# Performance work log

Measured on AMD Instinct MI355X. Metric: run time of the kernel, lower is better.

The kernel has to match this reference:

```python
import jax, jax.numpy as jnp
import numpy as np

B = 1048576  # number of Gaussians
EPS = 1e-8


def setup_inputs() -> dict:
    key = jax.random.key(0)
    ks = jax.random.split(key, 6)
    return {
        "loc1": jax.random.normal(ks[0], (B, 3), dtype=jnp.float32),
        "scale1": jax.random.uniform(ks[1], (B, 3), dtype=jnp.float32),
        "rot_matrix1": jax.random.normal(ks[2], (B, 3, 3), dtype=jnp.float32),
        "loc2": jax.random.normal(ks[3], (B, 3), dtype=jnp.float32),
        "scale2": jax.random.uniform(ks[4], (B, 3), dtype=jnp.float32),
        "rot_matrix2": jax.random.normal(ks[5], (B, 3, 3), dtype=jnp.float32),
    }


def reference(loc1, scale1, rot_matrix1, loc2, scale2, rot_matrix2):
    # Wasserstein-2 distance between batched 3D Gaussians.
    scale1 = jnp.clip(scale1, EPS)
    scale2 = jnp.clip(scale2, EPS)

    loc_diff2 = jnp.sum((loc1 - loc2) ** 2, axis=-1)  # [B]

    # cov2 = R2 diag(scale2) R2^T  -> [B,3,3]
    cov2 = jnp.einsum('bij,bj,bkj->bik', rot_matrix2, scale2, rot_matrix2)

    # cov2 rotated into frame 1: R1^T cov2 R1
    cov2_R1 = jnp.einsum('bji,bjk,bkl->bil', rot_matrix1, cov2, rot_matrix1)

    # E = diag(sqrt(scale1)) cov2_R1 diag(sqrt(scale1)), symmetrized
    s1_sqrt = jnp.sqrt(scale1)  # [B,3]
    E = s1_sqrt[:, :, None] * cov2_R1 * s1_sqrt[:, None, :]
    E = 0.5 * (E + jnp.swapaxes(E, -1, -2)) + EPS * jnp.eye(3, dtype=E.dtype)

    eigs = jnp.clip(jnp.linalg.eigvalsh(E), EPS)  # [B,3]
    E_sqrt_trace = jnp.sqrt(eigs).sum(axis=-1)  # [B]

    cov_w = (scale1.sum(axis=-1)
             + jnp.einsum('bii->b', cov2)
             - 2.0 * E_sqrt_trace)
    cov_w = jnp.clip(cov_w, 0.0)

    return jnp.sqrt(jnp.clip(loc_diff2 + cov_w, EPS))
```

## Files before the change

kernel.cpp:

```cpp
#include <hip/hip_runtime.h>
#include <math.h>

#define EPSF 1e-8f

__device__ __forceinline__ double tr_sqrt_eig(double a00, double a11, double a22,
                                              double a01, double a02, double a12)
{
    double q = (a00 + a11 + a22) * (1.0 / 3.0);
    double b00 = a00 - q, b11 = a11 - q, b22 = a22 - q;
    double p1 = a01 * a01 + a02 * a02 + a12 * a12;
    double p2 = b00 * b00 + b11 * b11 + b22 * b22 + 2.0 * p1;

    double e0, e1, e2;
    if (p2 <= 1e-30) {
        e0 = q; e1 = q; e2 = q;
    } else {
        double p = sqrt(p2 * (1.0 / 6.0));
        double invp = 1.0 / p;
        double c00 = b00 * invp, c11 = b11 * invp, c22 = b22 * invp;
        double c01 = a01 * invp, c02 = a02 * invp, c12 = a12 * invp;
        double detB = c00 * (c11 * c22 - c12 * c12)
                    - c01 * (c01 * c22 - c12 * c02)
                    + c02 * (c01 * c12 - c11 * c02);
        double r = 0.5 * detB;
        r = fmin(1.0, fmax(-1.0, r));
        double phi = acos(r) * (1.0 / 3.0);
        double twop = 2.0 * p;
        e0 = q + twop * cos(phi);
        e2 = q + twop * cos(phi + 2.0943951023931953);
        e1 = 3.0 * q - e0 - e2;
    }
    double eps_d = 1e-8;
    return sqrt(fmax(e0, eps_d)) + sqrt(fmax(e1, eps_d)) + sqrt(fmax(e2, eps_d));
}

__global__ __launch_bounds__(256) void wasserstein_kernel(
    const float* __restrict__ loc1, const float* __restrict__ scale1,
    const float* __restrict__ rot1, const float* __restrict__ loc2,
    const float* __restrict__ scale2, const float* __restrict__ rot2,
    float* __restrict__ out, int B4)
{
    int t = blockIdx.x * blockDim.x + threadIdx.x;
    if (t >= B4) return;

    const float4* l1p = (const float4*)loc1   + 3 * t;
    const float4* l2p = (const float4*)loc2   + 3 * t;
    const float4* s1p = (const float4*)scale1 + 3 * t;
    const float4* s2p = (const float4*)scale2 + 3 * t;
    const float4* r1p = (const float4*)rot1   + 9 * t;
    const float4* r2p = (const float4*)rot2   + 9 * t;

    float loc_diff2[4];
    {
        float L1[12], L2[12];
#pragma unroll
        for (int k = 0; k < 3; k++) {
            float4 a = l1p[k], b = l2p[k];
            L1[4 * k + 0] = a.x; L1[4 * k + 1] = a.y; L1[4 * k + 2] = a.z; L1[4 * k + 3] = a.w;
            L2[4 * k + 0] = b.x; L2[4 * k + 1] = b.y; L2[4 * k + 2] = b.z; L2[4 * k + 3] = b.w;
        }
#pragma unroll
        for (int g = 0; g < 4; g++) {
            float d0 = L1[3 * g + 0] - L2[3 * g + 0];
            float d1 = L1[3 * g + 1] - L2[3 * g + 1];
            float d2 = L1[3 * g + 2] - L2[3 * g + 2];
            loc_diff2[g] = d0 * d0 + d1 * d1 + d2 * d2;
        }
    }

    float cov2[4][6];
    float tr_cov2[4];
    {
        float S2[12], R2[36];
#pragma unroll
        for (int k = 0; k < 3; k++) {
            float4 v = s2p[k];
            S2[4 * k + 0] = v.x; S2[4 * k + 1] = v.y; S2[4 * k + 2] = v.z; S2[4 * k + 3] = v.w;
        }
#pragma unroll
        for (int k = 0; k < 9; k++) {
            float4 v = r2p[k];
            R2[4 * k + 0] = v.x; R2[4 * k + 1] = v.y; R2[4 * k + 2] = v.z; R2[4 * k + 3] = v.w;
        }
#pragma unroll
        for (int g = 0; g < 4; g++) {
            float s0 = fmaxf(S2[3 * g + 0], EPSF);
            float s1 = fmaxf(S2[3 * g + 1], EPSF);
            float s2 = fmaxf(S2[3 * g + 2], EPSF);
            const float* R = R2 + 9 * g;
            float c00 = R[0] * s0 * R[0] + R[1] * s1 * R[1] + R[2] * s2 * R[2];
            float c11 = R[3] * s0 * R[3] + R[4] * s1 * R[4] + R[5] * s2 * R[5];
            float c22 = R[6] * s0 * R[6] + R[7] * s1 * R[7] + R[8] * s2 * R[8];
            float c01 = R[0] * s0 * R[3] + R[1] * s1 * R[4] + R[2] * s2 * R[5];
            float c02 = R[0] * s0 * R[6] + R[1] * s1 * R[7] + R[2] * s2 * R[8];
            float c12 = R[3] * s0 * R[6] + R[4] * s1 * R[7] + R[5] * s2 * R[8];
            cov2[g][0] = c00; cov2[g][1] = c11; cov2[g][2] = c22;
            cov2[g][3] = c01; cov2[g][4] = c02; cov2[g][5] = c12;
            tr_cov2[g] = c00 + c11 + c22;
        }
    }

    float res[4];
    {
        float S1[12], R1[36];
#pragma unroll
        for (int k = 0; k < 3; k++) {
            float4 v = s1p[k];
            S1[4 * k + 0] = v.x; S1[4 * k + 1] = v.y; S1[4 * k + 2] = v.z; S1[4 * k + 3] = v.w;
        }
#pragma unroll
        for (int k = 0; k < 9; k++) {
            float4 v = r1p[k];
            R1[4 * k + 0] = v.x; R1[4 * k + 1] = v.y; R1[4 * k + 2] = v.z; R1[4 * k + 3] = v.w;
        }
#pragma unroll
        for (int g = 0; g < 4; g++) {
            float s0 = fmaxf(S1[3 * g + 0], EPSF);
            float s1 = fmaxf(S1[3 * g + 1], EPSF);
            float s2 = fmaxf(S1[3 * g + 2], EPSF);
            const float* R = R1 + 9 * g;
            float C[3][3];
            C[0][0] = cov2[g][0]; C[1][1] = cov2[g][1]; C[2][2] = cov2[g][2];
            C[0][1] = C[1][0] = cov2[g][3];
            C[0][2] = C[2][0] = cov2[g][4];
            C[1][2] = C[2][1] = cov2[g][5];

            float T[3][3];
#pragma unroll
            for (int r = 0; r < 3; r++)
#pragma unroll
                for (int c = 0; c < 3; c++)
                    T[r][c] = C[r][0] * R[c] + C[r][1] * R[3 + c] + C[r][2] * R[6 + c];

            float M[3][3];
#pragma unroll
            for (int r = 0; r < 3; r++)
#pragma unroll
                for (int c = 0; c < 3; c++)
                    M[r][c] = R[r] * T[0][c] + R[3 + r] * T[1][c] + R[6 + r] * T[2][c];

            float ss0 = sqrtf(s0), ss1 = sqrtf(s1), ss2 = sqrtf(s2);
            double a00 = (double)(s0 * M[0][0]) + 1e-8;
            double a11 = (double)(s1 * M[1][1]) + 1e-8;
            double a22 = (double)(s2 * M[2][2]) + 1e-8;
            double a01 = (double)(0.5f * (M[0][1] + M[1][0]) * ss0 * ss1);
            double a02 = (double)(0.5f * (M[0][2] + M[2][0]) * ss0 * ss2);
            double a12 = (double)(0.5f * (M[1][2] + M[2][1]) * ss1 * ss2);

            double trs = tr_sqrt_eig(a00, a11, a22, a01, a02, a12);

            float cov_w = (s0 + s1 + s2) + tr_cov2[g] - 2.0f * (float)trs;
            cov_w = fmaxf(cov_w, 0.0f);
            res[g] = sqrtf(fmaxf(loc_diff2[g] + cov_w, EPSF));
        }
    }

    float4 o;
    o.x = res[0]; o.y = res[1]; o.z = res[2]; o.w = res[3];
    ((float4*)out)[t] = o;
}

extern "C" void kernel_launch(void* const* d_in, const int* in_sizes, int n_in,
                              void* d_out, int out_size, void* d_ws, size_t ws_size,
                              hipStream_t stream) {
    const float* loc1   = (const float*)d_in[0];
    const float* scale1 = (const float*)d_in[1];
    const float* rot1   = (const float*)d_in[2];
    const float* loc2   = (const float*)d_in[3];
    const float* scale2 = (const float*)d_in[4];
    const float* rot2   = (const float*)d_in[5];
    float* out = (float*)d_out;

    int B = in_sizes[0] / 3;
    int B4 = B / 4;
    int block = 256;
    int grid = (B4 + block - 1) / block;
    wasserstein_kernel<<<grid, block, 0, stream>>>(loc1, scale1, rot1, loc2, scale2, rot2, out, B4);
}
```

Baseline: 157.9 us.

## Use float trig for eigenvalues and shrink block size to 64

Keeps the cubic invariants (q, p2, determinant) in double but takes acos/cos and the final square roots in single precision. It replaces the double sqrt and division with one rsqrt and folds the 1/p scaling into a cubed factor. The third eigenvalue is now computed directly from a cosine rather than from the trace. Block size and launch bounds drop from 256 to 64 threads. Double-precision transcendentals are expensive, so the aim is to cut ALU cost, at the risk of float-precision error in near-degenerate eigenvalue cases.

```diff
diff --git a/kernel.cpp b/kernel.cpp
--- a/kernel.cpp
+++ b/kernel.cpp
@@ -3,38 +3,37 @@
 
 #define EPSF 1e-8f
 
-__device__ __forceinline__ double tr_sqrt_eig(double a00, double a11, double a22,
-                                              double a01, double a02, double a12)
+__device__ __forceinline__ float tr_sqrt_eig(double a00, double a11, double a22,
+                                             double a01, double a02, double a12)
 {
     double q = (a00 + a11 + a22) * (1.0 / 3.0);
     double b00 = a00 - q, b11 = a11 - q, b22 = a22 - q;
     double p1 = a01 * a01 + a02 * a02 + a12 * a12;
     double p2 = b00 * b00 + b11 * b11 + b22 * b22 + 2.0 * p1;
 
-    double e0, e1, e2;
     if (p2 <= 1e-30) {
-        e0 = q; e1 = q; e2 = q;
-    } else {
-        double p = sqrt(p2 * (1.0 / 6.0));
-        double invp = 1.0 / p;
-        double c00 = b00 * invp, c11 = b11 * invp, c22 = b22 * invp;
-        double c01 = a01 * invp, c02 = a02 * invp, c12 = a12 * invp;
-        double detB = c00 * (c11 * c22 - c12 * c12)
-                    - c01 * (c01 * c22 - c12 * c02)
-                    + c02 * (c01 * c12 - c11 * c02);
-        double r = 0.5 * detB;
-        r = fmin(1.0, fmax(-1.0, r));
-        double phi = acos(r) * (1.0 / 3.0);
-        double twop = 2.0 * p;
-        e0 = q + twop * cos(phi);
-        e2 = q + twop * cos(phi + 2.0943951023931953);
-        e1 = 3.0 * q - e0 - e2;
+        return 3.0f * sqrtf(fmaxf((float)q, EPSF));
     }
-    double eps_d = 1e-8;
-    return sqrt(fmax(e0, eps_d)) + sqrt(fmax(e1, eps_d)) + sqrt(fmax(e2, eps_d));
+
+    double x = p2 * (1.0 / 6.0);
+    double inv = rsqrt(x);
+    double p = x * inv;
+    double detB = b00 * (b11 * b22 - a12 * a12)
+                - a01 * (a01 * b22 - a12 * a02)
+                + a02 * (a01 * a12 - b11 * a02);
+    double r = 0.5 * detB * (inv * inv * inv);
+    r = fmin(1.0, fmax(-1.0, r));
+
+    float phi = acosf((float)r) * (1.0f / 3.0f);
+    float qf = (float)q;
+    float tp = 2.0f * (float)p;
+    float e0 = qf + tp * cosf(phi);
+    float e1 = qf + tp * cosf(phi - 2.0943951023931953f);
+    float e2 = qf + tp * cosf(phi + 2.0943951023931953f);
+    return sqrtf(fmaxf(e0, EPSF)) + sqrtf(fmaxf(e1, EPSF)) + sqrtf(fmaxf(e2, EPSF));
 }
 
-__global__ __launch_bounds__(256) void wasserstein_kernel(
+__global__ __launch_bounds__(64) void wasserstein_kernel(
     const float* __restrict__ loc1, const float* __restrict__ scale1,
     const float* __restrict__ rot1, const float* __restrict__ loc2,
     const float* __restrict__ scale2, const float* __restrict__ rot2,
@@ -147,9 +146,9 @@
             double a02 = (double)(0.5f * (M[0][2] + M[2][0]) * ss0 * ss2);
             double a12 = (double)(0.5f * (M[1][2] + M[2][1]) * ss1 * ss2);
 
-            double trs = tr_sqrt_eig(a00, a11, a22, a01, a02, a12);
+            float trs = tr_sqrt_eig(a00, a11, a22, a01, a02, a12);
 
-            float cov_w = (s0 + s1 + s2) + tr_cov2[g] - 2.0f * (float)trs;
+            float cov_w = (s0 + s1 + s2) + tr_cov2[g] - 2.0f * trs;
             cov_w = fmaxf(cov_w, 0.0f);
             res[g] = sqrtf(fmaxf(loc_diff2[g] + cov_w, EPSF));
         }
@@ -173,7 +172,7 @@
 
     int B = in_sizes[0] / 3;
     int B4 = B / 4;
-    int block = 256;
+    int block = 64;
     int grid = (B4 + block - 1) / block;
     wasserstein_kernel<<<grid, block, 0, stream>>>(loc1, scale1, rot1, loc2, scale2, rot2, out, B4);
 }
```

After: 160.5 us. Within noise of the previous version (+1.6%).
